# Performance work log

Hardware: AMD Instinct MI355X
Metric: run time of the kernel (lower is better)

## Reference

```python
import jax, jax.numpy as jnp
import numpy as np

BITS = 4
PACK = 32 // BITS  # 8 nibbles per int32
GROUP = 128
MASK = (1 << BITS) - 1


def _dequant(qweight, qzeros, scales):
    # qweight: [K//8, N] int32, nibbles packed along K (input) dim
    # qzeros : [G, N//8] int32, nibbles packed along N (output) dim
    # scales : [G, N] float
    shifts = jnp.arange(PACK, dtype=jnp.int32) * BITS  # [8]
    Kp, N = qweight.shape
    G = scales.shape[0]
    # unpack weights along input dim -> [K, N]
    w = (qweight[:, None, :] >> shifts[None, :, None]) & MASK  # [K//8, 8, N]
    w = w.reshape(Kp * PACK, N).astype(scales.dtype)
    # unpack zeros along output dim -> [G, N]
    z = (qzeros[:, :, None] >> shifts[None, None, :]) & MASK  # [G, N//8, 8]
    z = z.reshape(G, N).astype(scales.dtype) + 1.0  # GPTQ +1 zero offset
    # broadcast per-group zero/scale over GROUP consecutive input rows
    z_full = jnp.repeat(z, GROUP, axis=0)       # [K, N]
    s_full = jnp.repeat(scales, GROUP, axis=0)  # [K, N]
    return (w - z_full) * s_full  # [K, N]


def setup_inputs() -> dict:
    key = jax.random.key(0)
    k1, k2, k3, k4 = jax.random.split(key, 4)
    K, N, T = 4096, 11008, 8192
    x = jax.random.normal(k1, (T, K), dtype=jnp.float32)
    qweight = jax.random.randint(k2, (K // PACK, N), 0, 2147483647, dtype=jnp.int32)
    qzeros = jax.random.randint(k3, (K // GROUP, N // PACK), 0, 2147483647, dtype=jnp.int32)
    scales = jax.random.uniform(k4, (K // GROUP, N), dtype=jnp.float32) * 0.01
    return {"x": x, "qweight": qweight, "qzeros": qzeros, "scales": scales}


def reference(x, qweight, qzeros, scales):
    W = _dequant(qweight, qzeros, scales)  # [K, N]
    return x @ W  # [T, N]
```

## Files before the change

### kernel.cpp

```cpp
#include <hip/hip_runtime.h>
#include <hip/hip_bf16.h>
#include <cstdint>
#include <cstddef>


#define K_DIM 4096
#define N_DIM 11008
#define GROUP_SZ 128
#define KB (K_DIM * 2)
#define NTILES_K (K_DIM / 64)

typedef __bf16 bf16x8_t __attribute__((ext_vector_type(8)));
typedef float f32x4_t __attribute__((ext_vector_type(4)));

__device__ __forceinline__ void async_copy16(const void* g, void* l) {
    __builtin_amdgcn_global_load_lds((const __attribute__((address_space(1))) void*)g,
                                     (__attribute__((address_space(3))) void*)l,
                                     16, 0, 0);
}

__global__ __launch_bounds__(256) void convert_x_kernel(const float* __restrict__ x,
                                                        __bf16* __restrict__ xb,
                                                        long total) {
    long i = ((long)blockIdx.x * 256 + threadIdx.x) * 8;
    if (i >= total) return;
    const float4* p = (const float4*)(x + i);
    float4 u = p[0], v = p[1];
    bf16x8_t o;
    o[0] = (__bf16)u.x; o[1] = (__bf16)u.y; o[2] = (__bf16)u.z; o[3] = (__bf16)u.w;
    o[4] = (__bf16)v.x; o[5] = (__bf16)v.y; o[6] = (__bf16)v.z; o[7] = (__bf16)v.w;
    *(bf16x8_t*)(xb + i) = o;
}

__global__ __launch_bounds__(256) void dequant_kernel(const int* __restrict__ qw,
                                                      const int* __restrict__ qz,
                                                      const float* __restrict__ sc,
                                                      __bf16* __restrict__ Wt) {
    __shared__ __align__(16) __bf16 dqT[128 * 136];
    __shared__ float dqS[128];
    __shared__ float dqB[128];
    const int n0 = blockIdx.x * 128;
    const int g  = blockIdx.y;
    const int t  = threadIdx.x;

    if (t < 128) {
        int n = n0 + t;
        float s = sc[(size_t)g * N_DIM + n];
        int z = (qz[(size_t)g * (N_DIM / 8) + (n >> 3)] >> ((n & 7) * 4)) & 15;
        dqS[t] = s;
        dqB[t] = -(float)(z + 1) * s;
    }
    __syncthreads();

#pragma unroll
    for (int it = 0; it < 8; ++it) {
        int wi  = it * 256 + t;
        int row = wi >> 7;
        int col = wi & 127;
        int q = qw[(size_t)(g * 16 + row) * N_DIM + n0 + col];
        float s = dqS[col], b = dqB[col];
        bf16x8_t v;
#pragma unroll
        for (int j = 0; j < 8; ++j) {
            float w = (float)((q >> (4 * j)) & 15);
            v[j] = (__bf16)fmaf(w, s, b);
        }
        *(bf16x8_t*)(&dqT[col * 136 + row * 8]) = v;
    }
    __syncthreads();

    int n_loc = t & 127, half = t >> 7;
    const __bf16* src = &dqT[n_loc * 136 + half * 64];
    __bf16* dst = Wt + (size_t)(n0 + n_loc) * K_DIM + g * GROUP_SZ + half * 64;
#pragma unroll
    for (int i = 0; i < 8; ++i)
        *(bf16x8_t*)(dst + i * 8) = *(const bf16x8_t*)(src + i * 8);
}

__global__ __launch_bounds__(512, 2) void gemm256_kernel(const __bf16* __restrict__ A,
                                                         const __bf16* __restrict__ Bt,
                                                         float* __restrict__ C,
                                                         int mtiles, int ntiles) {
    __shared__ __align__(16) char ldsA[2][256 * 128];
    __shared__ __align__(16) char ldsB[2][256 * 128];
    const int tid = threadIdx.x;

    const int nwg = gridDim.x;
    const int bid = blockIdx.x;
    int vid = (nwg & 7) ? bid : ((bid & 7) * (nwg >> 3) + (bid >> 3));
    int mt, nt;
    if ((mtiles & 15) == 0) {
        const int bandsz = 16 * ntiles;
        const int band = vid / bandsz, rem = vid % bandsz;
        nt = rem >> 4;
        mt = (band << 4) + (rem & 15);
    } else {
        mt = vid % mtiles;
        nt = vid / mtiles;
    }

    const char* aPanel = (const char*)A + (size_t)mt * 256 * KB;
    const char* bPanel = (const char*)Bt + (size_t)nt * 256 * KB;

    int srcA[2], srcB[2], dstA[2], dstB[2];
#pragma unroll
    for (int q = 0; q < 2; ++q) {
        const int f = q * 512 + tid;
        const int r = f >> 3, c = f & 7;
        const int swz = (c * 16) ^ ((r & 7) << 4);
        const int Ra = r + (r & 64);
        const int Rb = r + (r & ~31);
        srcA[q] = Ra * KB + swz;  dstA[q] = Ra * 128 + c * 16;
        srcB[q] = Rb * KB + swz;  dstB[q] = Rb * 128 + c * 16;
    }

    const int lane = tid & 63;
    const int wid = tid >> 6;
    const int wm = wid >> 2, wn = wid & 3;
    const int lr = lane & 15, lq = lane >> 4;
    const int kOff0 = (lq * 16) ^ ((lr & 7) << 4);
    const int kOff1 = (64 + lq * 16) ^ ((lr & 7) << 4);
    const int aRowBase = wm * 128 + lr;
    const int bRowBase = wn * 64 + lr;

    bf16x8_t aF[4][2], bF[4][2];
    f32x4_t acc[8][4];
#pragma unroll
    for (int m = 0; m < 8; ++m)
#pragma unroll
        for (int n = 0; n < 4; ++n)
            acc[m][n] = (f32x4_t){0.f, 0.f, 0.f, 0.f};

#define GL_A(KT, BUFS, ROFF) do {                                                          \
    async_copy16(aPanel + (size_t)(KT) * 128 + (ROFF) * KB + srcA[0],                      \
                 &ldsA[BUFS][(ROFF) * 128] + dstA[0]);                                     \
    async_copy16(aPanel + (size_t)(KT) * 128 + (ROFF) * KB + srcA[1],                      \
                 &ldsA[BUFS][(ROFF) * 128] + dstA[1]);                                     \
} while (0)
#define GL_B(KT, BUFS, ROFF) do {                                                          \
    async_copy16(bPanel + (size_t)(KT) * 128 + (ROFF) * KB + srcB[0],                      \
                 &ldsB[BUFS][(ROFF) * 128] + dstB[0]);                                     \
    async_copy16(bPanel + (size_t)(KT) * 128 + (ROFF) * KB + srcB[1],                      \
                 &ldsB[BUFS][(ROFF) * 128] + dstB[1]);                                     \
} while (0)
#define READ_A(MQ, BUFC) do {                                                              \
    _Pragma("unroll") for (int i = 0; i < 4; ++i) {                                        \
        const char* _p = &ldsA[BUFC][(aRowBase + (MQ) * 64 + i * 16) * 128];               \
        aF[i][0] = *(const bf16x8_t*)(_p + kOff0);                                         \
        aF[i][1] = *(const bf16x8_t*)(_p + kOff1);                                         \
    }                                                                                      \
} while (0)
#define READ_B(NQ, BUFC) do {                                                              \
    _Pragma("unroll") for (int j = 0; j < 2; ++j) {                                        \
        const char* _p = &ldsB[BUFC][(bRowBase + ((NQ) * 2 + j) * 16) * 128];              \
        bF[(NQ) * 2 + j][0] = *(const bf16x8_t*)(_p + kOff0);                              \
        bF[(NQ) * 2 + j][1] = *(const bf16x8_t*)(_p + kOff1);                              \
    }                                                                                      \
} while (0)
#define MFMA_QUAD(MQ, NQ) do {                                                             \
    _Pragma("unroll") for (int kk = 0; kk < 2; ++kk)                                       \
    _Pragma("unroll") for (int i = 0; i < 4; ++i)                                          \
    _Pragma("unroll") for (int j = 0; j < 2; ++j)                                          \
        acc[(MQ) * 4 + i][(NQ) * 2 + j] = __builtin_amdgcn_mfma_f32_16x16x32_bf16(         \
            aF[i][kk], bF[(NQ) * 2 + j][kk], acc[(MQ) * 4 + i][(NQ) * 2 + j], 0, 0, 0);    \
} while (0)
#define BARRIER() asm volatile("s_barrier" ::: "memory")
#define VMCNT4()  asm volatile("s_waitcnt vmcnt(4)" ::: "memory")

#define KTILE(BUFC, KTS) do {                                                              \
                                                                      \
    READ_A(0, BUFC); READ_B(0, BUFC);                                                      \
    GL_A(KTS, (BUFC) ^ 1, 0);                                                              \
    VMCNT4(); BARRIER();                                                                   \
    MFMA_QUAD(0, 0);                                                                       \
                                                                      \
    READ_B(1, BUFC);                                                                       \
    GL_B(KTS, (BUFC) ^ 1, 0);                                                              \
    VMCNT4(); BARRIER();                                                                   \
    MFMA_QUAD(0, 1);                                                                       \
                                                                      \
    READ_A(1, BUFC);                                                                       \
    GL_B(KTS, (BUFC) ^ 1, 32);                                                             \
    BARRIER();                                                                             \
    MFMA_QUAD(1, 1);                                                                       \
                                       \
    GL_A(KTS, (BUFC) ^ 1, 64);                                                             \
    VMCNT4(); BARRIER();                                                                   \
    MFMA_QUAD(1, 0);                                                                       \
} while (0)

    GL_A(0, 0, 0); GL_B(0, 0, 0); GL_B(0, 0, 32); GL_A(0, 0, 64);
    VMCNT4(); BARRIER();

#pragma unroll 1
    for (int kt = 0; kt < NTILES_K; kt += 2) {
        const int ks0 = kt + 1;
        const int ks1 = (kt + 2 < NTILES_K) ? kt + 2 : kt + 1;
        KTILE(0, ks0);
        KTILE(1, ks1);
    }

    asm volatile("s_waitcnt vmcnt(0)" ::: "memory");

#pragma unroll
    for (int m = 0; m < 8; ++m) {
        const size_t gr = (size_t)mt * 256 + wm * 128 + m * 16 + lq * 4;
#pragma unroll
        for (int n = 0; n < 4; ++n) {
            const size_t gc = (size_t)nt * 256 + wn * 64 + n * 16 + lr;
            float* cp = C + gr * N_DIM + gc;
#pragma unroll
            for (int rg = 0; rg < 4; ++rg)
                cp[(size_t)rg * N_DIM] = acc[m][n][rg];
        }
    }
}

__global__ __launch_bounds__(256) void fallback_kernel(const float* __restrict__ x,
                                                       const int* __restrict__ qw,
                                                       const int* __restrict__ qz,
                                                       const float* __restrict__ sc,
                                                       float* __restrict__ out) {
    __shared__ float xrow[K_DIM];
    const int t = blockIdx.y;
    const int n = blockIdx.x * 256 + threadIdx.x;
    for (int i = threadIdx.x; i < K_DIM; i += 256)
        xrow[i] = x[(size_t)t * K_DIM + i];
    __syncthreads();
    if (n >= N_DIM) return;
    float acc = 0.f;
    for (int g = 0; g < K_DIM / GROUP_SZ; ++g) {
        float s = sc[(size_t)g * N_DIM + n];
        int z = (qz[(size_t)g * (N_DIM / 8) + (n >> 3)] >> ((n & 7) * 4)) & 15;
        float b = -(float)(z + 1) * s;
        for (int kp = g * 16; kp < g * 16 + 16; ++kp) {
            int q = qw[(size_t)kp * N_DIM + n];
#pragma unroll
            for (int j = 0; j < 8; ++j) {
                float w = (float)((q >> (4 * j)) & 15);
                acc = fmaf(xrow[kp * 8 + j], fmaf(w, s, b), acc);
            }
        }
    }
    out[(size_t)t * N_DIM + n] = acc;
}

extern "C" void kernel_launch(void* const* d_in, const int* in_sizes, int n_in,
                              void* d_out, int out_size, void* d_ws, size_t ws_size,
                              hipStream_t stream) {
    const float* x  = (const float*)d_in[0];
    const int*   qw = (const int*)d_in[1];
    const int*   qz = (const int*)d_in[2];
    const float* sc = (const float*)d_in[3];
    float* out = (float*)d_out;

    const long T = (long)in_sizes[0] / K_DIM;
    const size_t xb_bytes = (size_t)T * K_DIM * sizeof(__bf16);
    const size_t wt_bytes = (size_t)N_DIM * K_DIM * sizeof(__bf16);

    if (ws_size >= xb_bytes + wt_bytes && (T % 256) == 0) {
        __bf16* xb = (__bf16*)d_ws;
        __bf16* Wt = (__bf16*)((char*)d_ws + xb_bytes);
        long total = T * K_DIM;
        long nthr = total / 8;
        convert_x_kernel<<<dim3((unsigned)((nthr + 255) / 256)), dim3(256), 0, stream>>>(x, xb, total);
        dequant_kernel<<<dim3(N_DIM / 128, K_DIM / GROUP_SZ), dim3(256), 0, stream>>>(qw, qz, sc, Wt);
        const int mtiles = (int)(T / 256);
        const int ntiles = N_DIM / 256;
        gemm256_kernel<<<dim3((unsigned)(mtiles * ntiles)), dim3(512), 0, stream>>>(xb, Wt, out, mtiles, ntiles);
    } else {
        fallback_kernel<<<dim3(N_DIM / 256 + 1, (unsigned)T), dim3(256), 0, stream>>>(x, qw, qz, sc, out);
    }
}
```

Before: 752.9 us.

## Make GEMM persistent with atomic tile scheduler and cross-tile prefetch

The GEMM kernel becomes persistent: a fixed grid of 256 workgroups pulls 256x256 output tiles from a global atomic counter. The counter is reset inside the convert kernel. While computing the last k-step of the current tile, each workgroup issues the loads for the next tile's first k-step, aiming to hide launch and prologue cost and tail effects. The catch is that the grid shrinks to one workgroup per CU despite launch bounds allowing two. Atomic ordering also replaces the XCD-aware block swizzle, which may hurt latency hiding and L2 locality.

Result: faster. 729.0 us (-3.2%).

```diff
diff --git a/kernel.cpp b/kernel.cpp
--- a/kernel.cpp
+++ b/kernel.cpp
@@ -21,7 +21,9 @@
 
 __global__ __launch_bounds__(256) void convert_x_kernel(const float* __restrict__ x,
                                                         __bf16* __restrict__ xb,
-                                                        long total) {
+                                                        long total,
+                                                        unsigned* __restrict__ counter) {
+    if (counter && blockIdx.x == 0 && threadIdx.x == 0) counter[0] = 0u;
     long i = ((long)blockIdx.x * 256 + threadIdx.x) * 8;
     if (i >= total) return;
     const float4* p = (const float4*)(x + i);
@@ -77,18 +79,8 @@
         *(bf16x8_t*)(dst + i * 8) = *(const bf16x8_t*)(src + i * 8);
 }
 
-__global__ __launch_bounds__(512, 2) void gemm256_kernel(const __bf16* __restrict__ A,
-                                                         const __bf16* __restrict__ Bt,
-                                                         float* __restrict__ C,
-                                                         int mtiles, int ntiles) {
-    __shared__ __align__(16) char ldsA[2][256 * 128];
-    __shared__ __align__(16) char ldsB[2][256 * 128];
-    const int tid = threadIdx.x;
-
-    const int nwg = gridDim.x;
-    const int bid = blockIdx.x;
-    int vid = (nwg & 7) ? bid : ((bid & 7) * (nwg >> 3) + (bid >> 3));
-    int mt, nt;
+__device__ __forceinline__ void map_tile(int vid, int mtiles, int ntiles,
+                                         int& mt, int& nt) {
     if ((mtiles & 15) == 0) {
         const int bandsz = 16 * ntiles;
         const int band = vid / bandsz, rem = vid % bandsz;
@@ -98,9 +90,17 @@
         mt = vid % mtiles;
         nt = vid / mtiles;
     }
-
-    const char* aPanel = (const char*)A + (size_t)mt * 256 * KB;
-    const char* bPanel = (const char*)Bt + (size_t)nt * 256 * KB;
+}
+
+__global__ __launch_bounds__(512, 2) void gemm256_kernel(const __bf16* __restrict__ A,
+                                                         const __bf16* __restrict__ Bt,
+                                                         float* __restrict__ C,
+                                                         int mtiles, int ntiles,
+                                                         unsigned* counter, int ntotal) {
+    __shared__ __align__(16) char ldsA[2][256 * 128];
+    __shared__ __align__(16) char ldsB[2][256 * 128];
+    __shared__ int sVid;
+    const int tid = threadIdx.x;
 
     int srcA[2], srcB[2], dstA[2], dstB[2];
 #pragma unroll
@@ -125,22 +125,17 @@
 
     bf16x8_t aF[4][2], bF[4][2];
     f32x4_t acc[8][4];
-#pragma unroll
-    for (int m = 0; m < 8; ++m)
-#pragma unroll
-        for (int n = 0; n < 4; ++n)
-            acc[m][n] = (f32x4_t){0.f, 0.f, 0.f, 0.f};
-
-#define GL_A(KT, BUFS, ROFF) do {                                                          \
-    async_copy16(aPanel + (size_t)(KT) * 128 + (ROFF) * KB + srcA[0],                      \
+
+#define GL_A(AP, KT, BUFS, ROFF) do {                                                      \
+    async_copy16((AP) + (size_t)(KT) * 128 + (ROFF) * KB + srcA[0],                        \
                  &ldsA[BUFS][(ROFF) * 128] + dstA[0]);                                     \
-    async_copy16(aPanel + (size_t)(KT) * 128 + (ROFF) * KB + srcA[1],                      \
+    async_copy16((AP) + (size_t)(KT) * 128 + (ROFF) * KB + srcA[1],                        \
                  &ldsA[BUFS][(ROFF) * 128] + dstA[1]);                                     \
 } while (0)
-#define GL_B(KT, BUFS, ROFF) do {                                                          \
-    async_copy16(bPanel + (size_t)(KT) * 128 + (ROFF) * KB + srcB[0],                      \
+#define GL_B(BP, KT, BUFS, ROFF) do {                                                      \
+    async_copy16((BP) + (size_t)(KT) * 128 + (ROFF) * KB + srcB[0],                        \
                  &ldsB[BUFS][(ROFF) * 128] + dstB[0]);                                     \
-    async_copy16(bPanel + (size_t)(KT) * 128 + (ROFF) * KB + srcB[1],                      \
+    async_copy16((BP) + (size_t)(KT) * 128 + (ROFF) * KB + srcB[1],                        \
                  &ldsB[BUFS][(ROFF) * 128] + dstB[1]);                                     \
 } while (0)
 #define READ_A(MQ, BUFC) do {                                                              \
@@ -166,53 +161,114 @@
 } while (0)
 #define BARRIER() asm volatile("s_barrier" ::: "memory")
 #define VMCNT4()  asm volatile("s_waitcnt vmcnt(4)" ::: "memory")
-
-#define KTILE(BUFC, KTS) do {                                                              \
-                                                                      \
+#define VMCNT0()  asm volatile("s_waitcnt vmcnt(0)" ::: "memory")
+
+#define KTILE(AP, BP, BUFC, KTS) do {                                                      \
     READ_A(0, BUFC); READ_B(0, BUFC);                                                      \
-    GL_A(KTS, (BUFC) ^ 1, 0);                                                              \
+    GL_A(AP, KTS, (BUFC) ^ 1, 0);                                                          \
     VMCNT4(); BARRIER();                                                                   \
     MFMA_QUAD(0, 0);                                                                       \
-                                                                      \
     READ_B(1, BUFC);                                                                       \
-    GL_B(KTS, (BUFC) ^ 1, 0);                                                              \
+    GL_B(BP, KTS, (BUFC) ^ 1, 0);                                                          \
     VMCNT4(); BARRIER();                                                                   \
     MFMA_QUAD(0, 1);                                                                       \
-                                                                      \
     READ_A(1, BUFC);                                                                       \
-    GL_B(KTS, (BUFC) ^ 1, 32);                                                             \
+    GL_B(BP, KTS, (BUFC) ^ 1, 32);                                                         \
     BARRIER();                                                                             \
     MFMA_QUAD(1, 1);                                                                       \
-                                       \
-    GL_A(KTS, (BUFC) ^ 1, 64);                                                             \
+    GL_A(AP, KTS, (BUFC) ^ 1, 64);                                                         \
     VMCNT4(); BARRIER();                                                                   \
     MFMA_QUAD(1, 0);                                                                       \
 } while (0)
 
-    GL_A(0, 0, 0); GL_B(0, 0, 0); GL_B(0, 0, 32); GL_A(0, 0, 64);
-    VMCNT4(); BARRIER();
+#define KTILE_LAST(NAP, NBP, HAVE) do {                                                    \
+    READ_A(0, 1); READ_B(0, 1);                                                            \
+    if (HAVE) { GL_A(NAP, 0, 0, 0); VMCNT4(); } else { VMCNT0(); }                         \
+    BARRIER();                                                                             \
+    MFMA_QUAD(0, 0);                                                                       \
+    READ_B(1, 1);                                                                          \
+    if (HAVE) GL_B(NBP, 0, 0, 0);                                                          \
+    VMCNT4(); BARRIER();                                                                   \
+    MFMA_QUAD(0, 1);                                                                       \
+    READ_A(1, 1);                                                                          \
+    if (HAVE) GL_B(NBP, 0, 0, 32);                                                         \
+    BARRIER();                                                                             \
+    MFMA_QUAD(1, 1);                                                                       \
+    if (HAVE) GL_A(NAP, 0, 0, 64);                                                         \
+    VMCNT4(); BARRIER();                                                                   \
+    MFMA_QUAD(1, 0);                                                                       \
+} while (0)
+
+    int vid;
+    if (counter) {
+        if (tid == 0) sVid = (int)atomicAdd(counter, 1u);
+        __syncthreads();
+        vid = sVid;
+    } else {
+        const int nwg = gridDim.x, bid = blockIdx.x;
+        vid = (nwg & 7) ? bid : ((bid & 7) * (nwg >> 3) + (bid >> 3));
+    }
+
+    bool first = true;
+    while (vid < ntotal) {
+        int mt, nt;
+        map_tile(vid, mtiles, ntiles, mt, nt);
+        const char* aPanel = (const char*)A + (size_t)mt * 256 * KB;
+        const char* bPanel = (const char*)Bt + (size_t)nt * 256 * KB;
+
+        if (first) {
+            GL_A(aPanel, 0, 0, 0); GL_B(bPanel, 0, 0, 0);
+            GL_B(bPanel, 0, 0, 32); GL_A(aPanel, 0, 0, 64);
+            VMCNT4(); BARRIER();
+            first = false;
+        }
+
+#pragma unroll
+        for (int m = 0; m < 8; ++m)
+#pragma unroll
+            for (int n = 0; n < 4; ++n)
+                acc[m][n] = (f32x4_t){0.f, 0.f, 0.f, 0.f};
 
 #pragma unroll 1
-    for (int kt = 0; kt < NTILES_K; kt += 2) {
-        const int ks0 = kt + 1;
-        const int ks1 = (kt + 2 < NTILES_K) ? kt + 2 : kt + 1;
-        KTILE(0, ks0);
-        KTILE(1, ks1);
-    }
-
-    asm volatile("s_waitcnt vmcnt(0)" ::: "memory");
-
-#pragma unroll
-    for (int m = 0; m < 8; ++m) {
-        const size_t gr = (size_t)mt * 256 + wm * 128 + m * 16 + lq * 4;
-#pragma unroll
-        for (int n = 0; n < 4; ++n) {
-            const size_t gc = (size_t)nt * 256 + wn * 64 + n * 16 + lr;
-            float* cp = C + gr * N_DIM + gc;
-#pragma unroll
-            for (int rg = 0; rg < 4; ++rg)
-                cp[(size_t)rg * N_DIM] = acc[m][n][rg];
-        }
+        for (int kt = 0; kt < NTILES_K - 2; kt += 2) {
+            KTILE(aPanel, bPanel, 0, kt + 1);
+            KTILE(aPanel, bPanel, 1, kt + 2);
+        }
+        KTILE(aPanel, bPanel, 0, NTILES_K - 1);
+
+        int nvid;
+        if (counter) {
+            if (tid == 0) sVid = (int)atomicAdd(counter, 1u);
+            __syncthreads();
+            nvid = sVid;
+        } else {
+            nvid = ntotal;
+        }
+        const bool have = nvid < ntotal;
+        const char* naP = aPanel;
+        const char* nbP = bPanel;
+        if (have) {
+            int nmt, nnt;
+            map_tile(nvid, mtiles, ntiles, nmt, nnt);
+            naP = (const char*)A + (size_t)nmt * 256 * KB;
+            nbP = (const char*)Bt + (size_t)nnt * 256 * KB;
+        }
+        KTILE_LAST(naP, nbP, have);
+
+#pragma unroll
+        for (int m = 0; m < 8; ++m) {
+            const size_t gr = (size_t)mt * 256 + wm * 128 + m * 16 + lq * 4;
+#pragma unroll
+            for (int n = 0; n < 4; ++n) {
+                const size_t gc = (size_t)nt * 256 + wn * 64 + n * 16 + lr;
+                float* cp = C + gr * N_DIM + gc;
+#pragma unroll
+                for (int rg = 0; rg < 4; ++rg)
+                    cp[(size_t)rg * N_DIM] = acc[m][n][rg];
+            }
+        }
+
+        vid = nvid;
     }
 }
 
@@ -257,17 +313,22 @@
     const long T = (long)in_sizes[0] / K_DIM;
     const size_t xb_bytes = (size_t)T * K_DIM * sizeof(__bf16);
     const size_t wt_bytes = (size_t)N_DIM * K_DIM * sizeof(__bf16);
+    const size_t cnt_off  = (xb_bytes + wt_bytes + 255) & ~(size_t)255;
 
     if (ws_size >= xb_bytes + wt_bytes && (T % 256) == 0) {
         __bf16* xb = (__bf16*)d_ws;
         __bf16* Wt = (__bf16*)((char*)d_ws + xb_bytes);
+        unsigned* counter = (ws_size >= cnt_off + 256)
+                          ? (unsigned*)((char*)d_ws + cnt_off) : nullptr;
         long total = T * K_DIM;
         long nthr = total / 8;
-        convert_x_kernel<<<dim3((unsigned)((nthr + 255) / 256)), dim3(256), 0, stream>>>(x, xb, total);
+        convert_x_kernel<<<dim3((unsigned)((nthr + 255) / 256)), dim3(256), 0, stream>>>(x, xb, total, counter);
         dequant_kernel<<<dim3(N_DIM / 128, K_DIM / GROUP_SZ), dim3(256), 0, stream>>>(qw, qz, sc, Wt);
         const int mtiles = (int)(T / 256);
         const int ntiles = N_DIM / 256;
-        gemm256_kernel<<<dim3((unsigned)(mtiles * ntiles)), dim3(512), 0, stream>>>(xb, Wt, out, mtiles, ntiles);
+        const int ntotal = mtiles * ntiles;
+        const unsigned grid = counter ? 256u : (unsigned)ntotal;
+        gemm256_kernel<<<dim3(grid), dim3(512), 0, stream>>>(xb, Wt, out, mtiles, ntiles, counter, ntotal);
     } else {
         fallback_kernel<<<dim3(N_DIM / 256 + 1, (unsigned)T), dim3(256), 0, stream>>>(x, qw, qz, sc, out);
     }
```
